# Kernel tuning notes

Hardware: AMD Instinct MI355X
Metric: run time of the kernel (lower is better)

The kernel has to match this reference:

```python
import jax, jax.numpy as jnp
import numpy as np

NUM_CLASSES = 80
NUM_ANCHORS = 5
ANCHORS = np.array([1.3221, 1.73145, 3.19275, 4.00944, 5.05587, 8.09892,
                    9.47112, 4.84053, 11.2364, 10.0071], dtype=np.float32).reshape(NUM_ANCHORS, 2)
COORD_SCALE = 1.0
NOOBJECT_SCALE = 1.0
OBJECT_SCALE = 5.0
CLASS_SCALE = 1.0
SIL_THRESH = 0.6
MAX_T = 50  # max ground-truth boxes per image
NB, NH, NW = 32, 38, 38


def bbox_iou(b1, b2):
    """IoU for center-format boxes (..., 4) = (cx, cy, w, h); broadcastable.
    Matches darknet bbox_ious with x1y1x2y2=False (zero IoU if no overlap)."""
    mx = jnp.minimum(b1[..., 0] - b1[..., 2] / 2, b2[..., 0] - b2[..., 2] / 2)
    Mx = jnp.maximum(b1[..., 0] + b1[..., 2] / 2, b2[..., 0] + b2[..., 2] / 2)
    my = jnp.minimum(b1[..., 1] - b1[..., 3] / 2, b2[..., 1] - b2[..., 3] / 2)
    My = jnp.maximum(b1[..., 1] + b1[..., 3] / 2, b2[..., 1] + b2[..., 3] / 2)
    cw = b1[..., 2] + b2[..., 2] - (Mx - mx)
    ch = b1[..., 3] + b2[..., 3] - (My - my)
    inter = jnp.where((cw > 0) & (ch > 0), cw * ch, 0.0)
    union = b1[..., 2] * b1[..., 3] + b2[..., 2] * b2[..., 3] - inter
    return inter / jnp.maximum(union, 1e-12)


def setup_inputs() -> dict:
    key = jax.random.key(0)
    k1, k2, k3 = jax.random.split(key, 3)
    output = jax.random.normal(k1, (NB, NUM_ANCHORS * (5 + NUM_CLASSES), NH, NW), dtype=jnp.float32)
    # target rows: 50 boxes x (cls, x, y, w, h), normalized coords in (0,1)
    target = jax.random.uniform(k2, (NB, MAX_T * 5), dtype=jnp.float32, minval=0.02, maxval=0.98)
    features = jax.random.normal(k3, (NB, 512, NH, NW), dtype=jnp.float32)
    return {"output": output, "target": target, "features": features}


def _region_loss(output, target):
    nB, _, nH, nW = output.shape
    nA, nC = NUM_ANCHORS, NUM_CLASSES
    anchors = jnp.asarray(ANCHORS)
    sg = jax.lax.stop_gradient

    out5 = output.reshape(nB, nA, 5 + nC, nH, nW)
    x = jax.nn.sigmoid(out5[:, :, 0])
    y = jax.nn.sigmoid(out5[:, :, 1])
    w = out5[:, :, 2]
    h = out5[:, :, 3]
    conf = jax.nn.sigmoid(out5[:, :, 4])
    cls = jnp.transpose(out5[:, :, 5:], (0, 1, 3, 4, 2))  # [nB,nA,nH,nW,nC]

    # predicted boxes in grid units (detached, as pred_boxes uses .data in torch)
    grid_x = jnp.arange(nW, dtype=output.dtype)
    grid_y = jnp.arange(nH, dtype=output.dtype)
    px = sg(x) + grid_x[None, None, None, :]
    py = sg(y) + grid_y[None, None, :, None]
    pw = jnp.exp(sg(w)) * anchors[None, :, 0, None, None]
    ph = jnp.exp(sg(h)) * anchors[None, :, 1, None, None]
    pred_boxes = jnp.stack([px, py, pw, ph], axis=-1)  # [nB,nA,nH,nW,4]

    tgt = sg(target).reshape(nB, MAX_T, 5)
    gx = tgt[..., 1] * nW
    gy = tgt[..., 2] * nH
    gw = tgt[..., 3] * nW
    gh = tgt[..., 4] * nH
    # original loop breaks at first target x == 0 -> valid prefix mask
    valid = jnp.cumprod((tgt[..., 1] != 0).astype(jnp.int32), axis=1).astype(bool)

    # ---- conf_mask silencing: max IoU of every predicted box vs any GT ----
    gt_boxes = jnp.stack([gx, gy, gw, gh], axis=-1)  # [nB,50,4]
    pb_flat = pred_boxes.reshape(nB, 1, nA * nH * nW, 4)
    ious = bbox_iou(gt_boxes[:, :, None, :], pb_flat)  # [nB,50,nA*nH*nW]
    max_iou = jnp.where(valid[:, :, None], ious, 0.0).max(axis=1).reshape(nB, nA, nH, nW)
    conf_mask = jnp.where(max_iou > SIL_THRESH, 0.0, NOOBJECT_SCALE).astype(output.dtype)

    # ---- seen < 12800 warm-up branch (self.seen = 0, anchor_step = 2) ----
    shp = (nB, nA, nH, nW)
    tx = jnp.full(shp, 0.5, output.dtype)
    ty = jnp.full(shp, 0.5, output.dtype)
    tw = jnp.zeros(shp, output.dtype)
    th = jnp.zeros(shp, output.dtype)
    coord_mask = jnp.ones(shp, output.dtype)
    cls_mask = jnp.zeros(shp, output.dtype)
    tconf = jnp.zeros(shp, output.dtype)
    tcls = jnp.zeros(shp, jnp.int32)

    # ---- best anchor per GT (IoU of wh-only boxes; argmax keeps first max,
    #      matching the strict '>' update in the loop) ----
    zeros = jnp.zeros_like(gw)
    gt_wh = jnp.stack([zeros, zeros, gw, gh], axis=-1)[:, :, None, :]  # [nB,50,1,4]
    anc_wh = jnp.concatenate([jnp.zeros_like(anchors), anchors], axis=-1)[None, None]  # [1,1,nA,4]
    best_n = jnp.argmax(bbox_iou(gt_wh, anc_wh), axis=-1)  # [nB,50]

    gi = jnp.clip(jnp.floor(gx).astype(jnp.int32), 0, nW - 1)
    gj = jnp.clip(jnp.floor(gy).astype(jnp.int32), 0, nH - 1)

    b_idx = jnp.arange(nB)[:, None]
    pbox = pred_boxes[b_idx, best_n, gj, gi]  # [nB,50,4]
    iou_gt = bbox_iou(gt_boxes, pbox)  # [nB,50]

    tx_val = gx - gi.astype(output.dtype)
    ty_val = gy - gj.astype(output.dtype)
    tw_val = jnp.log(jnp.maximum(gw, 1e-12) / anchors[best_n, 0])
    th_val = jnp.log(jnp.maximum(gh, 1e-12) / anchors[best_n, 1])
    cls_val = tgt[..., 0].astype(jnp.int32)

    bi = jnp.arange(nB)

    def step(carry, t):
        coord_m, conf_m, cls_m, tx, ty, tw, th, tconf, tcls = carry
        bn = best_n[:, t]
        j = gj[:, t]
        i = gi[:, t]
        v = valid[:, t]

        def upd(arr, val):
            # indices are distinct within one step (one GT per batch element)
            old = arr[bi, bn, j, i]
            return arr.at[bi, bn, j, i].set(jnp.where(v, val, old))

        coord_m = upd(coord_m, 1.0)
        cls_m = upd(cls_m, 1.0)
        conf_m = upd(conf_m, OBJECT_SCALE)
        tx = upd(tx, tx_val[:, t])
        ty = upd(ty, ty_val[:, t])
        tw = upd(tw, tw_val[:, t])
        th = upd(th, th_val[:, t])
        tconf = upd(tconf, iou_gt[:, t])
        tcls = upd(tcls, cls_val[:, t])
        return (coord_m, conf_m, cls_m, tx, ty, tw, th, tconf, tcls), None

    init = (coord_mask, conf_mask, cls_mask, tx, ty, tw, th, tconf, tcls)
    (coord_mask, conf_mask, cls_mask, tx, ty, tw, th, tconf, tcls), _ = jax.lax.scan(
        step, init, jnp.arange(MAX_T))

    conf_mask = jnp.sqrt(conf_mask)

    loss_x = COORD_SCALE * jnp.sum((x * coord_mask - tx * coord_mask) ** 2) / 2.0
    loss_y = COORD_SCALE * jnp.sum((y * coord_mask - ty * coord_mask) ** 2) / 2.0
    loss_w = COORD_SCALE * jnp.sum((w * coord_mask - tw * coord_mask) ** 2) / 2.0
    loss_h = COORD_SCALE * jnp.sum((h * coord_mask - th * coord_mask) ** 2) / 2.0
    loss_conf = jnp.sum((conf * conf_mask - tconf * conf_mask) ** 2) / 2.0

    # sum-reduced cross entropy over cells where cls_mask == 1
    logp = jax.nn.log_softmax(cls, axis=-1)
    picked = jnp.take_along_axis(logp, tcls[..., None], axis=-1)[..., 0]
    loss_cls = -CLASS_SCALE * jnp.sum(cls_mask * picked)

    return loss_x + loss_y + loss_w + loss_h + loss_conf + loss_cls


def reference(output, target, features):
    # `features` feeds the truncated adversarial-defense tail of the original
    # forward; the detection region loss below is the complete surviving math.
    return _region_loss(output, target)
```

## Files before the change

kernel.cpp:

```cpp
#include <hip/hip_runtime.h>
#include <math.h>

#define NB 32
#define NA 5
#define NC 80
#define NH 38
#define NW 38
#define MAXT 50
#define CELLS (NH * NW)
#define CH (5 + NC)
#define THREADS 256
#define NWAVES (THREADS / 64)
#define NCELLBLK 15
#define NCLSBLK 13
#define NXBLK (NCELLBLK + NCLSBLK)
#define NPAIRS 3610

__device__ float4 g_box[NB][MAXT];
__device__ float  g_thr[NB][MAXT];
__device__ int4   g_tgt[NB][MAXT];
__device__ float  g_corr[NB];
__device__ float  g_part[NB][NXBLK];

__device__ __constant__ float c_anchors[10] = {
    1.3221f, 1.73145f, 3.19275f, 4.00944f, 5.05587f,
    8.09892f, 9.47112f, 4.84053f, 11.2364f, 10.0071f};

__device__ __forceinline__ float sigmoidf_(float v) {
    return 1.0f / (1.0f + expf(-v));
}

__device__ __forceinline__ float bbox_iou_(float ax, float ay, float aw, float ah,
                                           float bx, float by, float bw, float bh) {
    float mx = fminf(ax - aw * 0.5f, bx - bw * 0.5f);
    float Mx = fmaxf(ax + aw * 0.5f, bx + bw * 0.5f);
    float my = fminf(ay - ah * 0.5f, by - bh * 0.5f);
    float My = fmaxf(ay + ah * 0.5f, by + bh * 0.5f);
    float cw = aw + bw - (Mx - mx);
    float ch = ah + bh - (My - my);
    float inter = (cw > 0.0f && ch > 0.0f) ? cw * ch : 0.0f;
    float uni = aw * ah + bw * bh - inter;
    return inter / fmaxf(uni, 1e-12f);
}

__device__ __forceinline__ bool hit50_(float px, float py, float pw, float ph,
                                       const float4* __restrict__ sb,
                                       const float* __restrict__ st) {
    float x1 = px - pw * 0.5f, x2 = px + pw * 0.5f;
    float y1 = py - ph * 0.5f, y2 = py + ph * 0.5f;
    float pthr = 0.375f * (pw * ph);
    bool hit = false;
    #pragma unroll
    for (int u = 0; u < MAXT; ++u) {
        float4 rb = sb[u];
        float ow = fminf(x2, rb.z) - fmaxf(x1, rb.x);
        float oh = fminf(y2, rb.w) - fmaxf(y1, rb.y);
        ow = fmaxf(ow, 0.0f);
        oh = fmaxf(oh, 0.0f);
        hit = hit | (ow * oh > pthr + st[u]);
    }
    return hit;
}

__device__ __forceinline__ float cell_loss_(float xr, float yr, float wr, float hr,
                                            float cr, int i, int j, int a,
                                            const float4* __restrict__ sb,
                                            const float* __restrict__ st) {
    float sx = sigmoidf_(xr), sy = sigmoidf_(yr), sc = sigmoidf_(cr);
    float px = sx + (float)i, py = sy + (float)j;
    float pw = expf(wr) * c_anchors[2 * a];
    float ph = expf(hr) * c_anchors[2 * a + 1];
    bool hit = hit50_(px, py, pw, ph, sb, st);
    float dx = sx - 0.5f, dy = sy - 0.5f;
    return 0.5f * (dx * dx + dy * dy + wr * wr + hr * hr)
         + (hit ? 0.0f : 0.5f * sc * sc);
}

__global__ __launch_bounds__(64) void region_prep(const float* __restrict__ out,
                                                  const float* __restrict__ tgt) {
    const int b = blockIdx.x;
    const int t = threadIdx.x;
    __shared__ float4 s_box[MAXT];
    __shared__ float  s_thr[MAXT];

    const bool isrec = (t < MAXT);
    float t0 = 0.f, t1 = 0.f, gx = 0.f, gy = 0.f, gw = 0.f, gh = 0.f;
    if (isrec) {
        const float* tp = tgt + (long)b * (MAXT * 5) + t * 5;
        t0 = tp[0];
        t1 = tp[1];
        gx = t1 * NW;
        gy = tp[2] * NH;
        gw = tp[3] * NW;
        gh = tp[4] * NH;
    }
    unsigned long long nz = __ballot(isrec && (t1 != 0.0f));
    bool valid = isrec && (((~nz) & ((2ULL << t) - 1ULL)) == 0ULL);

    int bn = 0;
    float best = -1.0f;
    for (int a = 0; a < NA; ++a) {
        float aw = c_anchors[2 * a], ah = c_anchors[2 * a + 1];
        float inter = fminf(gw, aw) * fminf(gh, ah);
        float uni = gw * gh + aw * ah - inter;
        float iou = inter / fmaxf(uni, 1e-12f);
        if (iou > best) { best = iou; bn = a; }
    }
    int gi = (int)floorf(gx); gi = gi < 0 ? 0 : (gi > NW - 1 ? NW - 1 : gi);
    int gj = (int)floorf(gy); gj = gj < 0 ? 0 : (gj > NH - 1 ? NH - 1 : gj);
    int key = valid ? (bn * CELLS + gj * NW + gi) : -1;

    unsigned long long eq = 0ULL;
    for (int u = 0; u < MAXT; ++u) {
        int ku = __shfl(key, u);
        eq |= (unsigned long long)(ku == key) << u;
    }
    bool winner = valid && ((eq & ~((2ULL << t) - 1ULL)) == 0ULL);

    float4 box;
    float thr;
    if (valid) {
        box.x = gx - gw * 0.5f; box.y = gy - gh * 0.5f;
        box.z = gx + gw * 0.5f; box.w = gy + gh * 0.5f;
        thr = 0.375f * (gw * gh);
    } else {
        box.x = box.y = box.z = box.w = 0.0f;
        thr = 3e38f;
    }
    if (isrec) {
        s_box[t] = box;
        s_thr[t] = thr;
        g_box[b][t] = box;
        g_thr[b][t] = thr;
        int cls = (int)t0; cls = cls < 0 ? 0 : (cls > NC - 1 ? NC - 1 : cls);
        int4 ti;
        ti.x = winner ? 1 : 0;
        ti.y = (bn * CH + 5) * CELLS + gj * NW + gi;
        ti.z = cls;
        ti.w = 0;
        g_tgt[b][t] = ti;
    }
    __syncthreads();

    float corr = 0.0f;
    if (winner) {
        float aw = c_anchors[2 * bn], ah = c_anchors[2 * bn + 1];
        long rb = (((long)(b * NA + bn)) * CH) * CELLS + gj * NW + gi;
        float xr = out[rb];
        float yr = out[rb + CELLS];
        float wr = out[rb + 2 * CELLS];
        float hr = out[rb + 3 * CELLS];
        float cr = out[rb + 4 * CELLS];
        float sx = sigmoidf_(xr), sy = sigmoidf_(yr), sc = sigmoidf_(cr);
        float px = sx + (float)gi, py = sy + (float)gj;
        float pw = expf(wr) * aw, ph = expf(hr) * ah;
        float iou_gt = bbox_iou_(gx, gy, gw, gh, px, py, pw, ph);
        bool rhit = hit50_(px, py, pw, ph, s_box, s_thr);
        float h01 = rhit ? 0.0f : 1.0f;

        float txv = gx - (float)gi, tyv = gy - (float)gj;
        float twv = logf(fmaxf(gw, 1e-12f) / aw);
        float thv = logf(fmaxf(gh, 1e-12f) / ah);
        float dsc = sc - iou_gt;
        corr = 0.5f * ((sx - txv) * (sx - txv) - (sx - 0.5f) * (sx - 0.5f)
                     + (sy - tyv) * (sy - tyv) - (sy - 0.5f) * (sy - 0.5f)
                     + (wr - twv) * (wr - twv) - wr * wr
                     + (hr - thv) * (hr - thv) - hr * hr)
             + 0.5f * (5.0f * dsc * dsc - h01 * sc * sc);
    }
    for (int off = 32; off > 0; off >>= 1) corr += __shfl_down(corr, off);
    if (t == 0) g_corr[b] = corr;
}

__global__ __launch_bounds__(THREADS) void region_main(const float* __restrict__ out) {
    const int bx = blockIdx.x;
    const int b = blockIdx.y;
    const int tid = threadIdx.x;
    const int wid = tid >> 6;
    const int lane = tid & 63;
    __shared__ float4 s_box[MAXT];
    __shared__ float  s_thr[MAXT];
    __shared__ float  s_wpart[NWAVES];

    if (bx < NCELLBLK) {
        const int p0 = bx * THREADS + tid;
        const int p = p0 < NPAIRS ? p0 : NPAIRS - 1;
        const int c0 = 2 * p;
        const int a = c0 / CELLS;
        const int r0 = c0 - a * CELLS;
        const int j = r0 / NW;
        const int i0 = r0 - j * NW;
        const long base = (((long)(b * NA + a)) * CH) * CELLS + r0;

        const float2 x2 = *(const float2*)&out[base];
        const float2 y2 = *(const float2*)&out[base + CELLS];
        const float2 w2 = *(const float2*)&out[base + 2 * CELLS];
        const float2 h2 = *(const float2*)&out[base + 3 * CELLS];
        const float2 q2 = *(const float2*)&out[base + 4 * CELLS];

        if (tid < MAXT) {
            s_box[tid] = g_box[b][tid];
            s_thr[tid] = g_thr[b][tid];
        }
        __syncthreads();

        float cs = cell_loss_(x2.x, y2.x, w2.x, h2.x, q2.x, i0,     j, a, s_box, s_thr)
                 + cell_loss_(x2.y, y2.y, w2.y, h2.y, q2.y, i0 + 1, j, a, s_box, s_thr);
        if (p0 >= NPAIRS) cs = 0.0f;

        for (int off = 32; off > 0; off >>= 1) cs += __shfl_down(cs, off);
        if (lane == 0) s_wpart[wid] = cs;
        __syncthreads();
        if (tid == 0) {
            float s = 0.0f;
            for (int w = 0; w < NWAVES; ++w) s += s_wpart[w];
            g_part[b][bx] = s;
        }
    } else {
        const int rec = __builtin_amdgcn_readfirstlane((bx - NCELLBLK) * NWAVES + wid);
        float closs = 0.0f;
        if (rec < MAXT) {
            const int4 ti = g_tgt[b][rec];
            if (ti.x) {
                const float* cp = out + (long)b * (NA * CH * CELLS) + ti.y;
                float v0 = cp[(long)lane * CELLS];
                float v1 = (lane < NC - 64) ? cp[(long)(64 + lane) * CELLS] : -INFINITY;
                float vc = cp[(long)ti.z * CELLS];
                float m = fmaxf(v0, v1);
                for (int off = 32; off > 0; off >>= 1)
                    m = fmaxf(m, __shfl_down(m, off));
                m = __shfl(m, 0);
                float e = expf(v0 - m) + ((lane < NC - 64) ? expf(v1 - m) : 0.0f);
                for (int off = 32; off > 0; off >>= 1)
                    e += __shfl_down(e, off);
                if (lane == 0) closs = m + logf(e) - vc;
            }
        }
        if (lane == 0) s_wpart[wid] = closs;
        __syncthreads();
        if (tid == 0) {
            float s = 0.0f;
            for (int w = 0; w < NWAVES; ++w) s += s_wpart[w];
            g_part[b][bx] = s;
        }
    }
}

__global__ __launch_bounds__(1024) void region_finish(float* __restrict__ loss) {
    const int tid = threadIdx.x;
    const int wid = tid >> 6;
    const int lane = tid & 63;
    __shared__ float sp[16];

    float v = 0.0f;
    if (tid < NB * NXBLK) v = ((const float*)g_part)[tid];
    if (tid < NB) v += g_corr[tid];

    for (int off = 32; off > 0; off >>= 1) v += __shfl_down(v, off);
    if (lane == 0) sp[wid] = v;
    __syncthreads();
    if (tid == 0) {
        float s = 0.0f;
        for (int w = 0; w < 16; ++w) s += sp[w];
        loss[0] = s;
    }
}

extern "C" void kernel_launch(void* const* d_in, const int* in_sizes, int n_in,
                              void* d_out, int out_size, void* d_ws, size_t ws_size,
                              hipStream_t stream) {
    const float* output = (const float*)d_in[0];
    const float* target = (const float*)d_in[1];
    float* loss = (float*)d_out;

    region_prep<<<NB, 64, 0, stream>>>(output, target);
    dim3 grid(NXBLK, NB);
    region_main<<<grid, THREADS, 0, stream>>>(output);
    region_finish<<<1, 1024, 0, stream>>>(loss);
}
```

Measured before the change: 176.0 us.

## Fuse target-prep kernel into main kernel, recomputing per-block target data

```diff
diff --git a/kernel.cpp b/kernel.cpp
--- a/kernel.cpp
+++ b/kernel.cpp
@@ -16,11 +16,7 @@
 #define NXBLK (NCELLBLK + NCLSBLK)
 #define NPAIRS 3610
 
-__device__ float4 g_box[NB][MAXT];
-__device__ float  g_thr[NB][MAXT];
-__device__ int4   g_tgt[NB][MAXT];
-__device__ float  g_corr[NB];
-__device__ float  g_part[NB][NXBLK];
+__device__ float g_part[NB][NXBLK];
 
 __device__ __constant__ float c_anchors[10] = {
     1.3221f, 1.73145f, 3.19275f, 4.00944f, 5.05587f,
@@ -76,173 +72,180 @@
          + (hit ? 0.0f : 0.5f * sc * sc);
 }
 
-__global__ __launch_bounds__(64) void region_prep(const float* __restrict__ out,
-                                                  const float* __restrict__ tgt) {
-    const int b = blockIdx.x;
-    const int t = threadIdx.x;
-    __shared__ float4 s_box[MAXT];
-    __shared__ float  s_thr[MAXT];
-
-    const bool isrec = (t < MAXT);
-    float t0 = 0.f, t1 = 0.f, gx = 0.f, gy = 0.f, gw = 0.f, gh = 0.f;
-    if (isrec) {
-        const float* tp = tgt + (long)b * (MAXT * 5) + t * 5;
-        t0 = tp[0];
-        t1 = tp[1];
-        gx = t1 * NW;
-        gy = tp[2] * NH;
-        gw = tp[3] * NW;
-        gh = tp[4] * NH;
-    }
-    unsigned long long nz = __ballot(isrec && (t1 != 0.0f));
-    bool valid = isrec && (((~nz) & ((2ULL << t) - 1ULL)) == 0ULL);
-
-    int bn = 0;
-    float best = -1.0f;
-    for (int a = 0; a < NA; ++a) {
-        float aw = c_anchors[2 * a], ah = c_anchors[2 * a + 1];
-        float inter = fminf(gw, aw) * fminf(gh, ah);
-        float uni = gw * gh + aw * ah - inter;
-        float iou = inter / fmaxf(uni, 1e-12f);
-        if (iou > best) { best = iou; bn = a; }
-    }
-    int gi = (int)floorf(gx); gi = gi < 0 ? 0 : (gi > NW - 1 ? NW - 1 : gi);
-    int gj = (int)floorf(gy); gj = gj < 0 ? 0 : (gj > NH - 1 ? NH - 1 : gj);
-    int key = valid ? (bn * CELLS + gj * NW + gi) : -1;
-
-    unsigned long long eq = 0ULL;
-    for (int u = 0; u < MAXT; ++u) {
-        int ku = __shfl(key, u);
-        eq |= (unsigned long long)(ku == key) << u;
-    }
-    bool winner = valid && ((eq & ~((2ULL << t) - 1ULL)) == 0ULL);
-
-    float4 box;
-    float thr;
-    if (valid) {
-        box.x = gx - gw * 0.5f; box.y = gy - gh * 0.5f;
-        box.z = gx + gw * 0.5f; box.w = gy + gh * 0.5f;
-        thr = 0.375f * (gw * gh);
-    } else {
-        box.x = box.y = box.z = box.w = 0.0f;
-        thr = 3e38f;
-    }
-    if (isrec) {
-        s_box[t] = box;
-        s_thr[t] = thr;
-        g_box[b][t] = box;
-        g_thr[b][t] = thr;
-        int cls = (int)t0; cls = cls < 0 ? 0 : (cls > NC - 1 ? NC - 1 : cls);
-        int4 ti;
-        ti.x = winner ? 1 : 0;
-        ti.y = (bn * CH + 5) * CELLS + gj * NW + gi;
-        ti.z = cls;
-        ti.w = 0;
-        g_tgt[b][t] = ti;
-    }
-    __syncthreads();
-
-    float corr = 0.0f;
-    if (winner) {
-        float aw = c_anchors[2 * bn], ah = c_anchors[2 * bn + 1];
-        long rb = (((long)(b * NA + bn)) * CH) * CELLS + gj * NW + gi;
-        float xr = out[rb];
-        float yr = out[rb + CELLS];
-        float wr = out[rb + 2 * CELLS];
-        float hr = out[rb + 3 * CELLS];
-        float cr = out[rb + 4 * CELLS];
-        float sx = sigmoidf_(xr), sy = sigmoidf_(yr), sc = sigmoidf_(cr);
-        float px = sx + (float)gi, py = sy + (float)gj;
-        float pw = expf(wr) * aw, ph = expf(hr) * ah;
-        float iou_gt = bbox_iou_(gx, gy, gw, gh, px, py, pw, ph);
-        bool rhit = hit50_(px, py, pw, ph, s_box, s_thr);
-        float h01 = rhit ? 0.0f : 1.0f;
-
-        float txv = gx - (float)gi, tyv = gy - (float)gj;
-        float twv = logf(fmaxf(gw, 1e-12f) / aw);
-        float thv = logf(fmaxf(gh, 1e-12f) / ah);
-        float dsc = sc - iou_gt;
-        corr = 0.5f * ((sx - txv) * (sx - txv) - (sx - 0.5f) * (sx - 0.5f)
-                     + (sy - tyv) * (sy - tyv) - (sy - 0.5f) * (sy - 0.5f)
-                     + (wr - twv) * (wr - twv) - wr * wr
-                     + (hr - thv) * (hr - thv) - hr * hr)
-             + 0.5f * (5.0f * dsc * dsc - h01 * sc * sc);
-    }
-    for (int off = 32; off > 0; off >>= 1) corr += __shfl_down(corr, off);
-    if (t == 0) g_corr[b] = corr;
-}
-
-__global__ __launch_bounds__(THREADS) void region_main(const float* __restrict__ out) {
+__global__ __launch_bounds__(THREADS) void region_main(const float* __restrict__ out,
+                                                       const float* __restrict__ tgt) {
     const int bx = blockIdx.x;
     const int b = blockIdx.y;
     const int tid = threadIdx.x;
     const int wid = tid >> 6;
     const int lane = tid & 63;
+    const bool isClass = (bx >= NCELLBLK);
+
     __shared__ float4 s_box[MAXT];
     __shared__ float  s_thr[MAXT];
+    __shared__ int    s_win[MAXT];
+    __shared__ int    s_off[MAXT];
+    __shared__ int    s_cls[MAXT];
+    __shared__ float  s_gx[MAXT], s_gy[MAXT], s_gw[MAXT], s_gh[MAXT];
+    __shared__ int    s_bn[MAXT], s_gi[MAXT], s_gj[MAXT];
     __shared__ float  s_wpart[NWAVES];
 
-    if (bx < NCELLBLK) {
-        const int p0 = bx * THREADS + tid;
-        const int p = p0 < NPAIRS ? p0 : NPAIRS - 1;
-        const int c0 = 2 * p;
-        const int a = c0 / CELLS;
-        const int r0 = c0 - a * CELLS;
-        const int j = r0 / NW;
-        const int i0 = r0 - j * NW;
+    float2 x2, y2, w2, h2, q2;
+    int a = 0, j = 0, i0 = 0, p0 = 0;
+    if (!isClass) {
+        p0 = bx * THREADS + tid;
+        int p = p0 < NPAIRS ? p0 : NPAIRS - 1;
+        int c0 = 2 * p;
+        a = c0 / CELLS;
+        int r0 = c0 - a * CELLS;
+        j = r0 / NW;
+        i0 = r0 - j * NW;
         const long base = (((long)(b * NA + a)) * CH) * CELLS + r0;
-
-        const float2 x2 = *(const float2*)&out[base];
-        const float2 y2 = *(const float2*)&out[base + CELLS];
-        const float2 w2 = *(const float2*)&out[base + 2 * CELLS];
-        const float2 h2 = *(const float2*)&out[base + 3 * CELLS];
-        const float2 q2 = *(const float2*)&out[base + 4 * CELLS];
-
-        if (tid < MAXT) {
-            s_box[tid] = g_box[b][tid];
-            s_thr[tid] = g_thr[b][tid];
-        }
-        __syncthreads();
-
+        x2 = *(const float2*)&out[base];
+        y2 = *(const float2*)&out[base + CELLS];
+        w2 = *(const float2*)&out[base + 2 * CELLS];
+        h2 = *(const float2*)&out[base + 3 * CELLS];
+        q2 = *(const float2*)&out[base + 4 * CELLS];
+    }
+
+    if (wid == 0) {
+        const bool isrec = (lane < MAXT);
+        float t0 = 0.f, t1 = 0.f, gx = 0.f, gy = 0.f, gw = 0.f, gh = 0.f;
+        if (isrec) {
+            const float* tp = tgt + (long)b * (MAXT * 5) + lane * 5;
+            t0 = tp[0];
+            t1 = tp[1];
+            gx = t1 * NW;
+            gy = tp[2] * NH;
+            gw = tp[3] * NW;
+            gh = tp[4] * NH;
+        }
+        unsigned long long nz = __ballot(isrec && (t1 != 0.0f));
+        bool valid = isrec && (((~nz) & ((2ULL << lane) - 1ULL)) == 0ULL);
+
+        float4 box;
+        float thr;
+        if (valid) {
+            box.x = gx - gw * 0.5f; box.y = gy - gh * 0.5f;
+            box.z = gx + gw * 0.5f; box.w = gy + gh * 0.5f;
+            thr = 0.375f * (gw * gh);
+        } else {
+            box.x = box.y = box.z = box.w = 0.0f;
+            thr = 3e38f;
+        }
+        if (isrec) {
+            s_box[lane] = box;
+            s_thr[lane] = thr;
+        }
+
+        if (isClass) {
+            int bn = 0;
+            float best = -1.0f;
+            for (int aa = 0; aa < NA; ++aa) {
+                float aw = c_anchors[2 * aa], ah = c_anchors[2 * aa + 1];
+                float inter = fminf(gw, aw) * fminf(gh, ah);
+                float uni = gw * gh + aw * ah - inter;
+                float iou = inter / fmaxf(uni, 1e-12f);
+                if (iou > best) { best = iou; bn = aa; }
+            }
+            int gi = (int)floorf(gx); gi = gi < 0 ? 0 : (gi > NW - 1 ? NW - 1 : gi);
+            int gj = (int)floorf(gy); gj = gj < 0 ? 0 : (gj > NH - 1 ? NH - 1 : gj);
+            int key = valid ? (bn * CELLS + gj * NW + gi) : -1;
+
+            unsigned long long eq = 0ULL;
+            for (int u = 0; u < MAXT; ++u) {
+                int ku = __shfl(key, u);
+                eq |= (unsigned long long)(ku == key) << u;
+            }
+            bool winner = valid && ((eq & ~((2ULL << lane) - 1ULL)) == 0ULL);
+
+            if (isrec) {
+                s_win[lane] = winner ? 1 : 0;
+                int cls = (int)t0; cls = cls < 0 ? 0 : (cls > NC - 1 ? NC - 1 : cls);
+                s_cls[lane] = cls;
+                s_off[lane] = (bn * CH + 5) * CELLS + gj * NW + gi;
+                s_gx[lane] = gx; s_gy[lane] = gy; s_gw[lane] = gw; s_gh[lane] = gh;
+                s_bn[lane] = bn; s_gi[lane] = gi; s_gj[lane] = gj;
+            }
+        }
+    }
+    __syncthreads();
+
+    if (!isClass) {
         float cs = cell_loss_(x2.x, y2.x, w2.x, h2.x, q2.x, i0,     j, a, s_box, s_thr)
                  + cell_loss_(x2.y, y2.y, w2.y, h2.y, q2.y, i0 + 1, j, a, s_box, s_thr);
         if (p0 >= NPAIRS) cs = 0.0f;
 
         for (int off = 32; off > 0; off >>= 1) cs += __shfl_down(cs, off);
         if (lane == 0) s_wpart[wid] = cs;
-        __syncthreads();
-        if (tid == 0) {
-            float s = 0.0f;
-            for (int w = 0; w < NWAVES; ++w) s += s_wpart[w];
-            g_part[b][bx] = s;
-        }
     } else {
         const int rec = __builtin_amdgcn_readfirstlane((bx - NCELLBLK) * NWAVES + wid);
         float closs = 0.0f;
-        if (rec < MAXT) {
-            const int4 ti = g_tgt[b][rec];
-            if (ti.x) {
-                const float* cp = out + (long)b * (NA * CH * CELLS) + ti.y;
-                float v0 = cp[(long)lane * CELLS];
-                float v1 = (lane < NC - 64) ? cp[(long)(64 + lane) * CELLS] : -INFINITY;
-                float vc = cp[(long)ti.z * CELLS];
-                float m = fmaxf(v0, v1);
-                for (int off = 32; off > 0; off >>= 1)
-                    m = fmaxf(m, __shfl_down(m, off));
-                m = __shfl(m, 0);
-                float e = expf(v0 - m) + ((lane < NC - 64) ? expf(v1 - m) : 0.0f);
-                for (int off = 32; off > 0; off >>= 1)
-                    e += __shfl_down(e, off);
-                if (lane == 0) closs = m + logf(e) - vc;
+        if (rec < MAXT && s_win[rec]) {
+            const int off_c = s_off[rec];
+            const int cls = s_cls[rec];
+            const float* cp = out + (long)b * (NA * CH * CELLS) + off_c;
+            float v0 = cp[(long)lane * CELLS];
+            float v1 = (lane < NC - 64) ? cp[(long)(64 + lane) * CELLS] : -INFINITY;
+            float vc = cp[(long)cls * CELLS];
+            float m = fmaxf(v0, v1);
+            for (int off = 32; off > 0; off >>= 1)
+                m = fmaxf(m, __shfl_down(m, off));
+            m = __shfl(m, 0);
+            float e = expf(v0 - m) + ((lane < NC - 64) ? expf(v1 - m) : 0.0f);
+            for (int off = 32; off > 0; off >>= 1)
+                e += __shfl_down(e, off);
+
+            float gx = s_gx[rec], gy = s_gy[rec], gw = s_gw[rec], gh = s_gh[rec];
+            int bn = s_bn[rec], gi = s_gi[rec], gj = s_gj[rec];
+            float aw = c_anchors[2 * bn], ah = c_anchors[2 * bn + 1];
+            long rb = (((long)(b * NA + bn)) * CH) * CELLS + gj * NW + gi;
+            float xr = out[rb];
+            float yr = out[rb + CELLS];
+            float wr = out[rb + 2 * CELLS];
+            float hr = out[rb + 3 * CELLS];
+            float cr = out[rb + 4 * CELLS];
+            float sx = sigmoidf_(xr), sy = sigmoidf_(yr), sc = sigmoidf_(cr);
+            float px = sx + (float)gi, py = sy + (float)gj;
+            float pw = expf(wr) * aw, ph = expf(hr) * ah;
+            float iou_gt = bbox_iou_(gx, gy, gw, gh, px, py, pw, ph);
+
+            float x1 = px - pw * 0.5f, xx2 = px + pw * 0.5f;
+            float y1 = py - ph * 0.5f, yy2 = py + ph * 0.5f;
+            float pthr = 0.375f * (pw * ph);
+            bool myhit = false;
+            if (lane < MAXT) {
+                float4 rbx = s_box[lane];
+                float ow = fminf(xx2, rbx.z) - fmaxf(x1, rbx.x);
+                float oh = fminf(yy2, rbx.w) - fmaxf(y1, rbx.y);
+                ow = fmaxf(ow, 0.0f);
+                oh = fmaxf(oh, 0.0f);
+                myhit = (ow * oh > pthr + s_thr[lane]);
+            }
+            bool rhit = (__ballot(myhit) != 0ULL);
+            float h01 = rhit ? 0.0f : 1.0f;
+
+            if (lane == 0) {
+                float txv = gx - (float)gi, tyv = gy - (float)gj;
+                float twv = logf(fmaxf(gw, 1e-12f) / aw);
+                float thv = logf(fmaxf(gh, 1e-12f) / ah);
+                float dsc = sc - iou_gt;
+                float corr = 0.5f * ((sx - txv) * (sx - txv) - (sx - 0.5f) * (sx - 0.5f)
+                                   + (sy - tyv) * (sy - tyv) - (sy - 0.5f) * (sy - 0.5f)
+                                   + (wr - twv) * (wr - twv) - wr * wr
+                                   + (hr - thv) * (hr - thv) - hr * hr)
+                           + 0.5f * (5.0f * dsc * dsc - h01 * sc * sc);
+                closs = (m + logf(e) - vc) + corr;
             }
         }
         if (lane == 0) s_wpart[wid] = closs;
-        __syncthreads();
-        if (tid == 0) {
-            float s = 0.0f;
-            for (int w = 0; w < NWAVES; ++w) s += s_wpart[w];
-            g_part[b][bx] = s;
-        }
+    }
+
+    __syncthreads();
+    if (tid == 0) {
+        float s = 0.0f;
+        for (int w = 0; w < NWAVES; ++w) s += s_wpart[w];
+        g_part[b][bx] = s;
     }
 }
 
@@ -254,7 +257,6 @@
 
     float v = 0.0f;
     if (tid < NB * NXBLK) v = ((const float*)g_part)[tid];
-    if (tid < NB) v += g_corr[tid];
 
     for (int off = 32; off > 0; off >>= 1) v += __shfl_down(v, off);
     if (lane == 0) sp[wid] = v;
@@ -273,8 +275,7 @@
     const float* target = (const float*)d_in[1];
     float* loss = (float*)d_out;
 
-    region_prep<<<NB, 64, 0, stream>>>(output, target);
     dim3 grid(NXBLK, NB);
-    region_main<<<grid, THREADS, 0, stream>>>(output);
+    region_main<<<grid, THREADS, 0, stream>>>(output, target);
     region_finish<<<1, 1024, 0, stream>>>(loss);
 }
```

Result: faster. 166.8 us (median of 2 runs) (-5.2%).
